# Kernel tuning notes

Hardware: AMD Instinct MI355X
Metric: run time of the kernel (lower is better)

## Reference

```python
import jax, jax.numpy as jnp
import numpy as np

N, D = 16384, 2048

def setup_inputs() -> dict:
    key = jax.random.key(0)
    k1, k2 = jax.random.split(key)
    F = jax.random.normal(k1, (N, D), dtype=jnp.float32)
    F_star = jax.random.normal(k2, (N, D), dtype=jnp.float32)
    lambda_r = jnp.float32(1.0)
    return {"F": F, "F_star": F_star, "lambda_r": lambda_r}

def reference(F, F_star, lambda_r):
    # trace(F F^T Fs Fs^T) == ||F^T Fs||_F^2 (cyclic trace property);
    # avoids materializing the n x n Gram matrices the torch code forms.
    G = jnp.einsum('nd,ne->de', F, F_star)  # [D, D]
    return lambda_r * jnp.sum(G * G)
```

## Files before the change

kernel.cpp:

```cpp
#include <hip/hip_runtime.h>
#include <hip/hip_bf16.h>

#define N_ROWS 16384
#define D_DIM  2048
#define SPLITK 4
#define NS     (N_ROWS / 32)
#define NP     (D_DIM / 128)
#define NSS    (NS / SPLITK)
#define NKT    (NSS / 2)


typedef __attribute__((ext_vector_type(8))) short short8;
typedef __attribute__((ext_vector_type(4))) float f32x4;
typedef __attribute__((ext_vector_type(8))) unsigned short ushort8;
typedef __attribute__((ext_vector_type(4))) unsigned short ushort4v;

#define GPTR(p) ((const __attribute__((address_space(1))) void*)(p))
#define LPTR(p) ((__attribute__((address_space(3))) void*)(p))

__device__ __forceinline__ unsigned short f2bf(float x) {
  __hip_bfloat16 b = __float2bfloat16(x);
  return *reinterpret_cast<unsigned short*>(&b);
}
__device__ __forceinline__ float bf2f(unsigned short u) {
  unsigned int v = ((unsigned int)u) << 16;
  return *reinterpret_cast<float*>(&v);
}

__global__ void __launch_bounds__(256) transpose_pack(
    const float* __restrict__ F, const float* __restrict__ Fs,
    unsigned short* __restrict__ Fb, unsigned short* __restrict__ Fsb) {
  const float* src = blockIdx.y ? Fs : F;
  unsigned short* dst = blockIdx.y ? Fsb : Fb;
  const int t = threadIdx.x;
  const int kb0 = blockIdx.x * 64;

  const int mg   = t & 31;
  const int koct = (t >> 5) & 3;
  const int c    = t >> 7;
  const int krow = kb0 + c * 32 + koct * 8;
  const int ks   = blockIdx.x * 2 + c;

  const float* srow = &src[(size_t)krow * D_DIM + mg * 4];
  unsigned short* obase = dst + (size_t)ks * 4096
                        + (size_t)(mg >> 2) * 512 + (size_t)koct * 128
                        + (size_t)(mg & 3) * 32;

#define STOREP(R, MT) do {                                                     \
    const float* _rp = (const float*)(R);                                      \
    unsigned short* _b = obase + (size_t)(MT) * (NS * 4096);                   \
    _Pragma("unroll") for (int i = 0; i < 4; ++i) {                            \
      ushort8 _o;                                                              \
      _Pragma("unroll") for (int j = 0; j < 8; ++j) _o[j] = f2bf(_rp[j*4+i]);  \
      *(ushort8*)&_b[i * 8] = _o;                                              \
    }                                                                          \
  } while (0)

  for (int mt = 0; mt < NP; mt += 2) {
    float4 r0[8], r1[8];
#pragma unroll
    for (int j = 0; j < 8; ++j) {
      r0[j] = *(const float4*)&srow[(size_t)j * D_DIM + mt * 128];
      r1[j] = *(const float4*)&srow[(size_t)j * D_DIM + mt * 128 + 128];
    }
    STOREP(r0, mt);
    STOREP(r1, mt + 1);
  }
#undef STOREP
}

__global__ void __launch_bounds__(512, 2) gemm_packed(
    const unsigned short* __restrict__ Fb, const unsigned short* __restrict__ Fsb,
    unsigned short* __restrict__ Cpart) {
  __shared__ unsigned short lds[65536];
  const int tid = threadIdx.x;
  const int w = tid >> 6, lane = tid & 63;
  const int wm = w >> 2, wn = w & 3;

  const int lin = blockIdx.x + (blockIdx.y << 3) + ((int)blockIdx.z << 6);
  const int l   = (lin & 7) * 32 + (lin >> 3);
  const int bx = l & 7, by = (l >> 3) & 7, z = l >> 6;

  const size_t kbase = (size_t)z * NSS * 4096;
  size_t aSrc0 = ((size_t)(by * 2 + 0) * NS) * 4096 + kbase + (size_t)w * 1024 + lane * 8;
  size_t aSrc1 = ((size_t)(by * 2 + 1) * NS) * 4096 + kbase + (size_t)w * 1024 + lane * 8;
  size_t bSrc0 = ((size_t)(bx * 2 + 0) * NS) * 4096 + kbase + (size_t)w * 1024 + lane * 8;
  size_t bSrc1 = ((size_t)(bx * 2 + 1) * NS) * 4096 + kbase + (size_t)w * 1024 + lane * 8;

  const int aRd = wm * 8192 + lane * 8;
  const int bRd = (wn >> 1) * 8192 + (wn & 1) * 2048 + lane * 8;

#define STAGE_A(KT, P, BUF) do {                                               \
    int _kt = (KT); if (_kt >= NKT) _kt -= NKT;                                \
    const unsigned short* _s = Fb + (P ? aSrc1 : aSrc0) + (size_t)_kt * 8192;  \
    unsigned short* _d = &lds[(BUF) * 16384 + (P) * 8192 + w * 1024];          \
    __builtin_amdgcn_global_load_lds(GPTR(_s),       LPTR(_d),       16, 0, 0);\
    __builtin_amdgcn_global_load_lds(GPTR(_s + 512), LPTR(_d + 512), 16, 0, 0);\
  } while (0)
#define STAGE_B(KT, Q, BUF) do {                                               \
    int _kt = (KT); if (_kt >= NKT) _kt -= NKT;                                \
    const unsigned short* _s = Fsb + (Q ? bSrc1 : bSrc0) + (size_t)_kt * 8192; \
    unsigned short* _d = &lds[32768 + (BUF) * 16384 + (Q) * 8192 + w * 1024];  \
    __builtin_amdgcn_global_load_lds(GPTR(_s),       LPTR(_d),       16, 0, 0);\
    __builtin_amdgcn_global_load_lds(GPTR(_s + 512), LPTR(_d + 512), 16, 0, 0);\
  } while (0)
#define LDA(DST, BUF, I, SL) (DST) = *(const short8*)&lds[(BUF) * 16384 + aRd + (SL) * 4096 + (I) * 512]
#define LDB(DST, BUF, J, SL) (DST) = *(const short8*)&lds[32768 + (BUF) * 16384 + bRd + (SL) * 4096 + (J) * 512]

  f32x4 acc[8][4];
#pragma unroll
  for (int i = 0; i < 8; ++i)
#pragma unroll
    for (int j = 0; j < 4; ++j) acc[i][j] = 0.f;

  short8 bAll[4][2];
  short8 aR[2][2][2];

  STAGE_A(0, 0, 0); STAGE_A(0, 1, 0);
  STAGE_B(0, 0, 0); STAGE_B(0, 1, 0);
  STAGE_B(1, 0, 1); STAGE_B(1, 1, 1);
  asm volatile("s_waitcnt vmcnt(4)" ::: "memory");
  __builtin_amdgcn_s_barrier();
  asm volatile("" ::: "memory");

#define TILE(T, B) do {                                                        \
    STAGE_A((T) + 1, 0, (B) ^ 1);                                              \
    STAGE_A((T) + 1, 1, (B) ^ 1);                                              \
    _Pragma("unroll") for (int j = 0; j < 4; ++j) {                            \
      LDB(bAll[j][0], B, j, 0); LDB(bAll[j][1], B, j, 1); }                    \
    LDA(aR[0][0][0], B, 0, 0); LDA(aR[0][0][1], B, 0, 1);                      \
    LDA(aR[0][1][0], B, 1, 0); LDA(aR[0][1][1], B, 1, 1);                      \
    _Pragma("unroll") for (int c = 0; c < 4; ++c) {                            \
      if (c < 3) {                                                             \
        LDA(aR[(c + 1) & 1][0][0], B, 2 * c + 2, 0);                           \
        LDA(aR[(c + 1) & 1][0][1], B, 2 * c + 2, 1);                           \
        LDA(aR[(c + 1) & 1][1][0], B, 2 * c + 3, 0);                           \
        LDA(aR[(c + 1) & 1][1][1], B, 2 * c + 3, 1);                           \
      }                                                                        \
      __builtin_amdgcn_s_setprio(1);                                           \
      _Pragma("unroll") for (int sl = 0; sl < 2; ++sl)                         \
        _Pragma("unroll") for (int iw = 0; iw < 2; ++iw)                       \
          _Pragma("unroll") for (int j = 0; j < 4; ++j)                        \
            acc[2 * c + iw][j] = __builtin_amdgcn_mfma_f32_16x16x32_bf16(      \
                aR[c & 1][iw][sl], bAll[j][sl], acc[2 * c + iw][j], 0, 0, 0);  \
      __builtin_amdgcn_s_setprio(0);                                           \
    }                                                                          \
    asm volatile("s_waitcnt lgkmcnt(0)" ::: "memory");                         \
    __builtin_amdgcn_s_barrier();                                              \
    asm volatile("" ::: "memory");                                             \
    STAGE_B((T) + 2, 0, B);                                                    \
    STAGE_B((T) + 2, 1, B);                                                    \
    asm volatile("s_waitcnt vmcnt(4)" ::: "memory");                           \
    __builtin_amdgcn_s_barrier();                                              \
    asm volatile("" ::: "memory");                                             \
  } while (0)

  for (int t = 0; t < NKT; t += 2) {
    TILE(t, 0);
    TILE(t + 1, 1);
  }

  unsigned short* cp = Cpart + (size_t)z * (D_DIM * D_DIM)
                     + (size_t)(by * 8 + bx) * 65536 + w * 8192 + lane * 4;
#pragma unroll
  for (int i = 0; i < 8; ++i)
#pragma unroll
    for (int j = 0; j < 4; ++j) {
      ushort4v o;
#pragma unroll
      for (int r = 0; r < 4; ++r) o[r] = f2bf(acc[i][j][r]);
      *(ushort4v*)&cp[(i * 4 + j) * 256] = o;
    }
#undef STAGE_A
#undef STAGE_B
#undef LDA
#undef LDB
#undef TILE
}

__global__ void __launch_bounds__(256) reduce_squares(
    const unsigned short* __restrict__ Cpart, const float* __restrict__ lam,
    float* __restrict__ out) {
  const int NQ = (D_DIM * D_DIM) / 8;
  const ushort8* c = (const ushort8*)Cpart;
  float s = 0.f;
  for (int idx = blockIdx.x * 256 + threadIdx.x; idx < NQ; idx += gridDim.x * 256) {
    float v[8];
#pragma unroll
    for (int j = 0; j < 8; ++j) v[j] = 0.f;
#pragma unroll
    for (int z = 0; z < SPLITK; ++z) {
      ushort8 u = c[(size_t)z * NQ + idx];
#pragma unroll
      for (int j = 0; j < 8; ++j) v[j] += bf2f(u[j]);
    }
#pragma unroll
    for (int j = 0; j < 8; ++j) s += v[j] * v[j];
  }
  for (int off = 32; off > 0; off >>= 1) s += __shfl_down(s, off, 64);
  __shared__ float red[4];
  const int wave = threadIdx.x >> 6, lane = threadIdx.x & 63;
  if (lane == 0) red[wave] = s;
  __syncthreads();
  if (threadIdx.x == 0) atomicAdd(out, (red[0] + red[1] + red[2] + red[3]) * lam[0]);
}

__global__ void __launch_bounds__(256) fallback_kernel(
    const float* __restrict__ F, const float* __restrict__ Fs,
    const float* __restrict__ lam, float* __restrict__ out) {
  __shared__ float sA[64][16], sB[64][16];
  const int d0 = blockIdx.y * 16, e0 = blockIdx.x * 16;
  const int t = threadIdx.x;
  const int td = t >> 4, te = t & 15;
  float s = 0.f;
  for (int k0 = 0; k0 < N_ROWS; k0 += 64) {
#pragma unroll
    for (int p = 0; p < 4; ++p) {
      const int k = (t >> 4) + p * 16;
      const int cc = t & 15;
      sA[k][cc] = F[(size_t)(k0 + k) * D_DIM + d0 + cc];
      sB[k][cc] = Fs[(size_t)(k0 + k) * D_DIM + e0 + cc];
    }
    __syncthreads();
#pragma unroll
    for (int kk = 0; kk < 64; ++kk) s += sA[kk][td] * sB[kk][te];
    __syncthreads();
  }
  float q = s * s;
  for (int off = 32; off > 0; off >>= 1) q += __shfl_down(q, off, 64);
  __shared__ float red[4];
  if ((t & 63) == 0) red[t >> 6] = q;
  __syncthreads();
  if (t == 0) atomicAdd(out, (red[0] + red[1] + red[2] + red[3]) * lam[0]);
}

extern "C" void kernel_launch(void* const* d_in, const int* in_sizes, int n_in,
                              void* d_out, int out_size, void* d_ws, size_t ws_size,
                              hipStream_t stream) {
  const float* F   = (const float*)d_in[0];
  const float* Fs  = (const float*)d_in[1];
  const float* lam = (const float*)d_in[2];
  float* out = (float*)d_out;
  hipMemsetAsync(d_out, 0, sizeof(float) * (size_t)out_size, stream);

  const size_t bf_bytes = (size_t)NP * NS * 8192;
  const size_t cpart_bytes = (size_t)SPLITK * D_DIM * D_DIM * 2;
  const size_t need = 2 * bf_bytes + cpart_bytes;

  if (ws_size >= need) {
    unsigned short* Fb  = (unsigned short*)d_ws;
    unsigned short* Fsb = Fb + bf_bytes / 2;
    unsigned short* Cpart = (unsigned short*)((char*)d_ws + 2 * bf_bytes);
    transpose_pack<<<dim3(N_ROWS / 64, 2), 256, 0, stream>>>(F, Fs, Fb, Fsb);
    gemm_packed<<<dim3(8, 8, SPLITK), 512, 0, stream>>>(Fb, Fsb, Cpart);
    reduce_squares<<<dim3(1024), 256, 0, stream>>>(Cpart, lam, out);
  } else {
    fallback_kernel<<<dim3(128, 128), 256, 0, stream>>>(F, Fs, lam, out);
  }
}
```

Measured before the change: 435.0 us.

## Stage transpose-pack through LDS for coalesced reads and wide packed stores

Rewrites the fp32-to-bf16 transpose/pack kernel so each block reads 32 full-width rows with coalesced float4 loads into shared memory, then re-reads column pairs from LDS and emits 16-byte packed stores in the MFMA tile layout. The grid grows to one block per 32-row k-slab per half of D per input, which raises parallelism. The goal is better global memory coalescing and higher bandwidth in the conversion pass, at the cost of 64KB of LDS per block, which limits occupancy.

```diff
diff --git a/kernel.cpp b/kernel.cpp
--- a/kernel.cpp
+++ b/kernel.cpp
@@ -30,43 +30,47 @@
 __global__ void __launch_bounds__(256) transpose_pack(
     const float* __restrict__ F, const float* __restrict__ Fs,
     unsigned short* __restrict__ Fb, unsigned short* __restrict__ Fsb) {
-  const float* src = blockIdx.y ? Fs : F;
-  unsigned short* dst = blockIdx.y ? Fsb : Fb;
+  __shared__ unsigned short kl[32 * 1024];
+  const float* src = blockIdx.z ? Fs : F;
+  unsigned short* dst = blockIdx.z ? Fsb : Fb;
   const int t = threadIdx.x;
-  const int kb0 = blockIdx.x * 64;
-
-  const int mg   = t & 31;
-  const int koct = (t >> 5) & 3;
-  const int c    = t >> 7;
-  const int krow = kb0 + c * 32 + koct * 8;
-  const int ks   = blockIdx.x * 2 + c;
-
-  const float* srow = &src[(size_t)krow * D_DIM + mg * 4];
-  unsigned short* obase = dst + (size_t)ks * 4096
-                        + (size_t)(mg >> 2) * 512 + (size_t)koct * 128
-                        + (size_t)(mg & 3) * 32;
-
-#define STOREP(R, MT) do {                                                     \
-    const float* _rp = (const float*)(R);                                      \
-    unsigned short* _b = obase + (size_t)(MT) * (NS * 4096);                   \
-    _Pragma("unroll") for (int i = 0; i < 4; ++i) {                            \
-      ushort8 _o;                                                              \
-      _Pragma("unroll") for (int j = 0; j < 8; ++j) _o[j] = f2bf(_rp[j*4+i]);  \
-      *(ushort8*)&_b[i * 8] = _o;                                              \
-    }                                                                          \
-  } while (0)
-
-  for (int mt = 0; mt < NP; mt += 2) {
-    float4 r0[8], r1[8];
-#pragma unroll
-    for (int j = 0; j < 8; ++j) {
-      r0[j] = *(const float4*)&srow[(size_t)j * D_DIM + mt * 128];
-      r1[j] = *(const float4*)&srow[(size_t)j * D_DIM + mt * 128 + 128];
-    }
-    STOREP(r0, mt);
-    STOREP(r1, mt + 1);
-  }
-#undef STOREP
+  const int ks = blockIdx.x;
+  const int half = blockIdx.y;
+
+  const float* sbase = src + (size_t)(ks * 32) * D_DIM + half * 1024 + t * 4;
+#pragma unroll
+  for (int k = 0; k < 32; ++k) {
+    float4 v = *(const float4*)(sbase + (size_t)k * D_DIM);
+    ushort4v o;
+    o[0] = f2bf(v.x); o[1] = f2bf(v.y); o[2] = f2bf(v.z); o[3] = f2bf(v.w);
+    *(ushort4v*)&kl[k * 1024 + t * 4] = o;
+  }
+  __syncthreads();
+
+  const unsigned int* kl32 = (const unsigned int*)kl;
+#pragma unroll
+  for (int q = 0; q < 2; ++q) {
+    const int p = t + 256 * q;
+    const int m0 = half * 1024 + 2 * p;
+    const int mt = m0 >> 7, tt = (m0 >> 4) & 7, mf = m0 & 15;
+    unsigned short* ob = dst + ((size_t)mt * NS + ks) * 4096 + tt * 512 + mf * 8;
+#pragma unroll
+    for (int koct = 0; koct < 4; ++koct) {
+      unsigned int r[8];
+#pragma unroll
+      for (int j = 0; j < 8; ++j) r[j] = kl32[(koct * 8 + j) * 512 + p];
+      ushort8 oA, oB;
+      unsigned int* a32 = (unsigned int*)&oA;
+      unsigned int* b32 = (unsigned int*)&oB;
+#pragma unroll
+      for (int i = 0; i < 4; ++i) {
+        a32[i] = (r[2 * i] & 0xFFFFu) | (r[2 * i + 1] << 16);
+        b32[i] = (r[2 * i] >> 16) | (r[2 * i + 1] & 0xFFFF0000u);
+      }
+      *(ushort8*)&ob[koct * 128] = oA;
+      *(ushort8*)&ob[koct * 128 + 8] = oB;
+    }
+  }
 }
 
 __global__ void __launch_bounds__(512, 2) gemm_packed(
@@ -251,7 +255,7 @@
     unsigned short* Fb  = (unsigned short*)d_ws;
     unsigned short* Fsb = Fb + bf_bytes / 2;
     unsigned short* Cpart = (unsigned short*)((char*)d_ws + 2 * bf_bytes);
-    transpose_pack<<<dim3(N_ROWS / 64, 2), 256, 0, stream>>>(F, Fs, Fb, Fsb);
+    transpose_pack<<<dim3(NS, 2, 2), 256, 0, stream>>>(F, Fs, Fb, Fsb);
     gemm_packed<<<dim3(8, 8, SPLITK), 512, 0, stream>>>(Fb, Fsb, Cpart);
     reduce_squares<<<dim3(1024), 256, 0, stream>>>(Cpart, lam, out);
   } else {
```

Result: faster. 415.5 us (-4.5%).
